# Kernel optimization log

Measured on AMD Instinct MI355X. Metric: run time of the kernel, lower is better.

Reference implementation:

```python
import jax, jax.numpy as jnp
import numpy as np

B, S, D, H = 4, 2048, 1024, 16
HD = D // H  # head_dim = 64


def setup_inputs() -> dict:
    key = jax.random.key(0)
    ks = jax.random.split(key, 8)
    scale = 1.0 / np.sqrt(D)
    return {
        "hidden_states": jax.random.normal(ks[0], (B, S, D), dtype=jnp.float32),
        "attention_mask": jnp.zeros((B, 1, 1, S), dtype=jnp.float32),
        "Wq": jax.random.normal(ks[1], (D, D), dtype=jnp.float32) * scale,
        "bq": jnp.zeros((D,), dtype=jnp.float32),
        "Wk": jax.random.normal(ks[2], (D, D), dtype=jnp.float32) * scale,
        "bk": jnp.zeros((D,), dtype=jnp.float32),
        "Wv": jax.random.normal(ks[3], (D, D), dtype=jnp.float32) * scale,
        "bv": jnp.zeros((D,), dtype=jnp.float32),
    }


def reference(hidden_states, attention_mask, Wq, bq, Wk, bk, Wv, bv):
    def split_heads(x):
        # [B,S,D] -> [B,H,S,HD]
        return x.reshape(B, S, H, HD).transpose(0, 2, 1, 3)

    q = split_heads(hidden_states @ Wq + bq)
    k = split_heads(hidden_states @ Wk + bk)
    v = split_heads(hidden_states @ Wv + bv)

    # [B,H,S,S]
    scores = jnp.einsum("bhqd,bhkd->bhqk", q, k) / jnp.sqrt(jnp.float32(HD))
    scores = scores + attention_mask  # additive mask, broadcasts [B,1,1,S]
    probs = jax.nn.softmax(scores, axis=-1)

    ctx = jnp.einsum("bhqk,bhkd->bhqd", probs, v)  # [B,H,S,HD]
    return ctx.transpose(0, 2, 1, 3).reshape(B, S, D)
```

## Files before the change

kernel.cpp:

```cpp
#include <hip/hip_runtime.h>
#include <hip/hip_bf16.h>
#include <stdint.h>

typedef __attribute__((ext_vector_type(4))) float f32x4;
typedef __attribute__((ext_vector_type(16))) float f32x16;
typedef __attribute__((ext_vector_type(8))) short bf16x8;
typedef __attribute__((ext_vector_type(4))) int int4v;
typedef __attribute__((ext_vector_type(8))) unsigned short u16x8;
typedef unsigned int u32;

static __device__ __forceinline__ unsigned short f2bf(float f) {
    union { float f; unsigned u; } v; v.f = f;
    unsigned r = v.u + 0x7FFF + ((v.u >> 16) & 1);
    return (unsigned short)(r >> 16);
}

static __device__ __forceinline__ u32 cvtpk(float lo, float hi) {
    u32 r;
    asm("v_cvt_pk_bf16_f32 %0, %1, %2" : "=v"(r) : "v"(lo), "v"(hi));
    return r;
}

static __device__ __forceinline__ void pl32swap_u(u32& a, u32& b) {
    asm("v_permlane32_swap_b32 %0, %1" : "+v"(a), "+v"(b));
}

static __device__ __forceinline__ void gload16(const void* g, void* lds) {
    __builtin_amdgcn_global_load_lds((const __attribute__((address_space(1))) void*)g,
                                     (__attribute__((address_space(3))) void*)lds,
                                     16, 0, 0);
}

__global__ __launch_bounds__(256) void cvt_x_kernel(const float* __restrict__ x,
                                                    unsigned short* __restrict__ xb) {
    int i = (blockIdx.x * 256 + threadIdx.x) * 4;
    float4 v = *(const float4*)(x + i);
    ushort4 o = make_ushort4(f2bf(v.x), f2bf(v.y), f2bf(v.z), f2bf(v.w));
    *(ushort4*)(xb + i) = o;
}

__global__ __launch_bounds__(256) void cvt_w_kernel(const float* __restrict__ Wq,
                                                    const float* __restrict__ Wk,
                                                    const float* __restrict__ Wv,
                                                    unsigned short* __restrict__ Wt3) {
    const float* W = (blockIdx.z == 0) ? Wq : ((blockIdx.z == 1) ? Wk : Wv);
    unsigned short* out = Wt3 + (size_t)blockIdx.z * 1024 * 1024;
    __shared__ unsigned short t[64][68];
    int k0 = blockIdx.x * 64, n0 = blockIdx.y * 64;
    int tid = threadIdx.x;
#pragma unroll
    for (int i = 0; i < 4; i++) {
        int c = i * 256 + tid;
        int row = c >> 4, cb = c & 15;
        float4 v = *(const float4*)(W + (size_t)(k0 + row) * 1024 + n0 + cb * 4);
        ushort4 o = make_ushort4(f2bf(v.x), f2bf(v.y), f2bf(v.z), f2bf(v.w));
        *(ushort4*)(&t[row][cb * 4]) = o;
    }
    __syncthreads();
#pragma unroll
    for (int i = 0; i < 2; i++) {
        int c = i * 256 + tid;
        int n = c >> 3, kc = c & 7;
        u16x8 tmp;
#pragma unroll
        for (int j = 0; j < 8; j++) tmp[j] = t[kc * 8 + j][n];
        *(u16x8*)(&out[(size_t)(n0 + n) * 1024 + k0 + kc * 8]) = tmp;
    }
}

__global__ __launch_bounds__(256) void mask_reorder_kernel(const float* __restrict__ mask,
                                                           float* __restrict__ maskr) {
    int o = blockIdx.x * 256 + threadIdx.x;
    int reg = o & 15, kvb = (o >> 4) & 1, hi2 = (o >> 5) & 1, kt = (o >> 6) & 31, bb = o >> 11;
    int kv = kt * 64 + kvb * 32 + (reg & 3) + 8 * (reg >> 2) + 4 * hi2;
    maskr[o] = 8.0f * mask[bb * 2048 + kv];
}

__global__ __launch_bounds__(256) void qkv_gemm_kernel(
    const unsigned short* __restrict__ Xb,
    const unsigned short* __restrict__ Wt3,
    const float* __restrict__ bq, const float* __restrict__ bk, const float* __restrict__ bv,
    unsigned short* __restrict__ Qo, unsigned short* __restrict__ Ko,
    unsigned short* __restrict__ Vt)
{
    int z = blockIdx.z;
    const unsigned short* Wt = Wt3 + (size_t)z * 1048576;
    const float* bias = (z == 0) ? bq : ((z == 1) ? bk : bv);
    int m0 = blockIdx.x * 128, n0 = blockIdx.y * 128;

    __shared__ __align__(16) unsigned short As[128 * 64];
    __shared__ __align__(16) unsigned short Bs[128 * 64];

    int tid = threadIdx.x, lane = tid & 63, wave = tid >> 6;
    int wm = wave >> 1, wn = wave & 1;
    int lr = lane & 15, lg = lane >> 4;

    const int chunkrow = lane >> 3, colp = (lane & 7) * 8;
    const unsigned short* aBase = Xb + (size_t)(m0 + wave * 32 + chunkrow) * 1024 + colp;
    const unsigned short* bBase = Wt + (size_t)(n0 + wave * 32 + chunkrow) * 1024 + colp;
    char* lA = (char*)As + wave * 4096;
    char* lB = (char*)Bs + wave * 4096;

    f32x4 acc[4][4] = {};

    for (int kt = 0; kt < 16; kt++) {
        int kbase = kt * 64;
#pragma unroll
        for (int c = 0; c < 4; c++) {
            gload16(aBase + kbase + c * 8192, lA + c * 1024);
            gload16(bBase + kbase + c * 8192, lB + c * 1024);
        }
        __syncthreads();
#pragma unroll
        for (int kk = 0; kk < 2; kk++) {
            bf16x8 a[4], bb[4];
#pragma unroll
            for (int mi = 0; mi < 4; mi++)
                a[mi] = *(const bf16x8*)((char*)As + (wm * 64 + mi * 16 + lr) * 128 + kk * 64 + lg * 16);
#pragma unroll
            for (int ni = 0; ni < 4; ni++)
                bb[ni] = *(const bf16x8*)((char*)Bs + (wn * 64 + ni * 16 + lr) * 128 + kk * 64 + lg * 16);
#pragma unroll
            for (int mi = 0; mi < 4; mi++)
#pragma unroll
                for (int ni = 0; ni < 4; ni++)
                    acc[mi][ni] = __builtin_amdgcn_mfma_f32_16x16x32_bf16(a[mi], bb[ni], acc[mi][ni], 0, 0, 0);
        }
        __syncthreads();
    }

    if (z < 2) {
        unsigned short* out = (z == 0) ? Qo : Ko;
#pragma unroll
        for (int ni = 0; ni < 4; ni++) {
            int n = n0 + wn * 64 + ni * 16 + lr;
            float bsv = bias[n];
#pragma unroll
            for (int mi = 0; mi < 4; mi++) {
                int mrow = m0 + wm * 64 + mi * 16 + lg * 4;
#pragma unroll
                for (int r = 0; r < 4; r++)
                    out[(size_t)(mrow + r) * 1024 + n] = f2bf(acc[mi][ni][r] + bsv);
            }
        }
    } else {
#pragma unroll
        for (int ni = 0; ni < 4; ni++) {
            int n = n0 + wn * 64 + ni * 16 + lr;
            float bsv = bias[n];
            int h = n >> 6, hd = n & 63;
#pragma unroll
            for (int mi = 0; mi < 4; mi++) {
                int mrow = m0 + wm * 64 + mi * 16 + lg * 4;
                int b = mrow >> 11, s = mrow & 2047;
                ushort4 pk = make_ushort4(f2bf(acc[mi][ni][0] + bsv),
                                          f2bf(acc[mi][ni][1] + bsv),
                                          f2bf(acc[mi][ni][2] + bsv),
                                          f2bf(acc[mi][ni][3] + bsv));
                *(ushort4*)(&Vt[((size_t)(b * 16 + h) * 64 + hd) * 2048 + s]) = pk;
            }
        }
    }
}

__global__ __launch_bounds__(256) void attn_kernel(
    const unsigned short* __restrict__ Q,
    const unsigned short* __restrict__ K,
    const unsigned short* __restrict__ Vt,
    const float* __restrict__ maskr,
    float* __restrict__ out)
{
    __shared__ __align__(16) char smem[33280];
    const int tid = threadIdx.x, lane = tid & 63, w = tid >> 6;
    const int ln31 = lane & 31, hi = lane >> 5;
    const int bh = blockIdx.y, b = bh >> 4, h = bh & 15;
    const int q0 = blockIdx.x * 128 + w * 32;
    const int swz = (ln31 & 7) << 4;
    const float c1 = 0.18033688011112042f;

    const unsigned short* Qrow = Q + (size_t)(b * 2048 + q0 + ln31) * 1024 + h * 64;
    bf16x8 aq[4];
#pragma unroll
    for (int ds = 0; ds < 4; ds++) aq[ds] = *(const bf16x8*)(Qrow + ds * 16 + hi * 8);

    const unsigned short* Kbp = K + (size_t)b * 2048 * 1024 + h * 64;
    const unsigned short* Vbp = Vt + (size_t)bh * 64 * 2048;

    const int r0 = tid >> 3, cb = tid & 7;
    const int woff = r0 * 128 + ((cb * 16) ^ ((r0 & 7) << 4));

    const unsigned short* kp = Kbp + (size_t)r0 * 1024 + cb * 8;
    const unsigned short* vp = Vbp + (size_t)r0 * 2048 + cb * 8;
    const float* mp = maskr + (size_t)b * 2048 + tid * 4;

    f32x16 oacc0 = {}, oacc1 = {};
    float mc = 8.0f * c1;
    float lrun = 0.f;

    int4v kr0, kr1, vr0, vr1, mr = {};
    kr0 = *(const int4v*)kp; kr1 = *(const int4v*)(kp + 32 * 1024);
    vr0 = *(const int4v*)vp; vr1 = *(const int4v*)(vp + 32 * 2048);
    if (tid < 16) mr = *(const int4v*)mp;
    kp += 65536; vp += 64; mp += 64;
    *(int4v*)(smem + woff) = kr0;
    *(int4v*)(smem + 32 * 128 + woff) = kr1;
    *(int4v*)(smem + 16384 + woff) = vr0;
    *(int4v*)(smem + 16384 + 32 * 128 + woff) = vr1;
    if (tid < 16) *(int4v*)(smem + 32768 + tid * 16) = mr;
    kr0 = *(const int4v*)kp; kr1 = *(const int4v*)(kp + 32 * 1024);
    vr0 = *(const int4v*)vp; vr1 = *(const int4v*)(vp + 32 * 2048);
    if (tid < 16) mr = *(const int4v*)mp;
    kp += 65536; vp += 64; mp += 64;
    __syncthreads();

#pragma unroll 2
    for (int kt = 0; kt < 32; kt++) {
        const int cur = kt & 1;
        const char* KsL = smem + cur * 8192 + ln31 * 128;
        const char* VsL = KsL + 16384;
        const f32x4* mpl = (const f32x4*)(smem + 32768 + cur * 256 + hi * 128);

        f32x16 st0, st1;
        {
            f32x4 a0 = mpl[0], a1 = mpl[1], a2 = mpl[2], a3 = mpl[3];
            f32x4 a4 = mpl[4], a5 = mpl[5], a6 = mpl[6], a7 = mpl[7];
#pragma unroll
            for (int j = 0; j < 4; j++) {
                st0[j] = a0[j]; st0[4 + j] = a1[j]; st0[8 + j] = a2[j]; st0[12 + j] = a3[j];
                st1[j] = a4[j]; st1[4 + j] = a5[j]; st1[8 + j] = a6[j]; st1[12 + j] = a7[j];
            }
        }

        __builtin_amdgcn_s_setprio(1);
#pragma unroll
        for (int ds = 0; ds < 4; ds++) {
            const int co = (ds * 32 + hi * 16) ^ swz;
            bf16x8 ka0 = *(const bf16x8*)(KsL + co);
            bf16x8 ka1 = *(const bf16x8*)(KsL + 4096 + co);
            st0 = __builtin_amdgcn_mfma_f32_32x32x16_bf16(ka0, aq[ds], st0, 0, 0, 0);
            st1 = __builtin_amdgcn_mfma_f32_32x32x16_bf16(ka1, aq[ds], st1, 0, 0, 0);
        }
        __builtin_amdgcn_s_setprio(0);

        if (kt < 31) {
            char* base = smem + (cur ^ 1) * 8192;
            *(int4v*)(base + woff) = kr0;
            *(int4v*)(base + 32 * 128 + woff) = kr1;
            *(int4v*)(base + 16384 + woff) = vr0;
            *(int4v*)(base + 16384 + 32 * 128 + woff) = vr1;
            if (tid < 16) *(int4v*)(smem + 32768 + (cur ^ 1) * 256 + tid * 16) = mr;
            if (kt < 30) {
                kr0 = *(const int4v*)kp; kr1 = *(const int4v*)(kp + 32 * 1024);
                vr0 = *(const int4v*)vp; vr1 = *(const int4v*)(vp + 32 * 2048);
                if (tid < 16) mr = *(const int4v*)mp;
                kp += 65536; vp += 64; mp += 64;
            }
        }

        float s16[16];
#pragma unroll
        for (int j = 0; j < 16; j++) {
            float v0 = __builtin_amdgcn_exp2f(__builtin_fmaf(st0[j], c1, -mc));
            float v1 = __builtin_amdgcn_exp2f(__builtin_fmaf(st1[j], c1, -mc));
            st0[j] = v0; st1[j] = v1; s16[j] = v0 + v1;
        }
#pragma unroll
        for (int stp = 8; stp > 0; stp >>= 1)
#pragma unroll
            for (int j = 0; j < 8; j++) if (j < stp) s16[j] += s16[j + stp];

        if (__any(s16[0] > 256.0f)) {
            float me = st0[0];
#pragma unroll
            for (int j = 1; j < 16; j++) me = fmaxf(me, st0[j]);
#pragma unroll
            for (int j = 0; j < 16; j++) me = fmaxf(me, st1[j]);
            me = fmaxf(me, __shfl_xor(me, 32));
            me = fmaxf(me, 1.0f);
            const float al = 1.0f / me;
            mc += __log2f(me);
            lrun *= al; s16[0] *= al;
#pragma unroll
            for (int j = 0; j < 16; j++) {
                st0[j] *= al; st1[j] *= al;
                oacc0[j] *= al; oacc1[j] *= al;
            }
        }
        lrun += s16[0];

        __builtin_amdgcn_s_setprio(1);
#pragma unroll
        for (int s = 0; s < 4; s++) {
            const f32x16& pp = (s & 2) ? st1 : st0;
            const int rA = (s & 1) * 8, rB = rA + 4;
            u32 w0 = cvtpk(pp[rA + 0], pp[rA + 1]);
            u32 w1 = cvtpk(pp[rA + 2], pp[rA + 3]);
            u32 w2 = cvtpk(pp[rB + 0], pp[rB + 1]);
            u32 w3 = cvtpk(pp[rB + 2], pp[rB + 3]);
            pl32swap_u(w0, w2);
            pl32swap_u(w1, w3);
            union { u32 u[4]; bf16x8 v; } pb;
            pb.u[0] = w0; pb.u[1] = w1; pb.u[2] = w2; pb.u[3] = w3;
            const int co = (s * 32 + hi * 16) ^ swz;
            bf16x8 va0 = *(const bf16x8*)(VsL + co);
            bf16x8 va1 = *(const bf16x8*)(VsL + 4096 + co);
            oacc0 = __builtin_amdgcn_mfma_f32_32x32x16_bf16(va0, pb.v, oacc0, 0, 0, 0);
            oacc1 = __builtin_amdgcn_mfma_f32_32x32x16_bf16(va1, pb.v, oacc1, 0, 0, 0);
        }
        __builtin_amdgcn_s_setprio(0);

        __syncthreads();
    }

    float lt = lrun + __shfl_xor(lrun, 32);
    const float rl = 1.0f / lt;
    float* lw = (float*)(smem + w * 4096);
    const int qp = lane >> 1, hb = (lane & 1) * 16;
#pragma unroll
    for (int p = 0; p < 2; p++) {
        const f32x16& oa = p ? oacc1 : oacc0;
#pragma unroll
        for (int r = 0; r < 16; r++) {
            int hd = (r & 3) + 8 * (r >> 2) + 4 * hi;
            lw[hd * 32 + ln31] = oa[r] * rl;
        }
        float* od = out + (size_t)(b * 2048 + q0 + qp) * 1024 + h * 64 + p * 32 + hb;
#pragma unroll
        for (int c = 0; c < 4; c++) {
            f32x4 o4;
#pragma unroll
            for (int j = 0; j < 4; j++) o4[j] = lw[(hb + c * 4 + j) * 32 + qp];
            *(f32x4*)(od + c * 4) = o4;
        }
        __syncthreads();
    }
}

extern "C" void kernel_launch(void* const* d_in, const int* in_sizes, int n_in,
                              void* d_out, int out_size, void* d_ws, size_t ws_size,
                              hipStream_t stream) {
    const float* hs   = (const float*)d_in[0];
    const float* mask = (const float*)d_in[1];
    const float* Wq   = (const float*)d_in[2];
    const float* bq   = (const float*)d_in[3];
    const float* Wk   = (const float*)d_in[4];
    const float* bk   = (const float*)d_in[5];
    const float* Wv   = (const float*)d_in[6];
    const float* bv   = (const float*)d_in[7];
    float* out = (float*)d_out;

    char* ws = (char*)d_ws;
    unsigned short* Xb  = (unsigned short*)ws;
    unsigned short* Wt3 = (unsigned short*)(ws + 16777216);
    unsigned short* Qb  = (unsigned short*)(ws + 16777216 + 6291456);
    unsigned short* Kb  = Qb + 8388608;
    unsigned short* Vt  = Kb + 8388608;
    float* maskr = (float*)(ws + 16777216 + 6291456 + 3 * 16777216);

    cvt_x_kernel<<<8192, 256, 0, stream>>>(hs, Xb);
    cvt_w_kernel<<<dim3(16, 16, 3), 256, 0, stream>>>(Wq, Wk, Wv, Wt3);
    mask_reorder_kernel<<<32, 256, 0, stream>>>(mask, maskr);
    qkv_gemm_kernel<<<dim3(64, 8, 3), 256, 0, stream>>>(Xb, Wt3, bq, bk, bv, Qb, Kb, Vt);
    attn_kernel<<<dim3(16, 64), 256, 0, stream>>>(Qb, Kb, Vt, maskr, out);
}
```

Measured before the change: 199.9 us.

## Double-buffer QKV GEMM LDS tiles and remap block IDs for XCD locality

Converts the QKV projection GEMM from a single 64-wide K tile with two barriers per iteration into a double-buffered 32-wide K tile pipeline. The next tile's global-to-LDS load is issued while the current tile is being consumed by MFMAs, leaving one barrier per step. It also remaps the linear block ID so that consecutive blocks on each XCD (bid&7 striding) cover contiguous tiles, aiming for better L2 reuse of X and W. Risks are halved MFMA work per barrier and possible LDS bank conflicts with the 64-byte row stride.

New measurement: 213.9 us. 7.0% more time.

```diff
diff --git a/kernel.cpp b/kernel.cpp
--- a/kernel.cpp
+++ b/kernel.cpp
@@ -83,51 +83,62 @@
     unsigned short* __restrict__ Qo, unsigned short* __restrict__ Ko,
     unsigned short* __restrict__ Vt)
 {
-    int z = blockIdx.z;
+    const int bid = blockIdx.x + 64 * blockIdx.y + 512 * blockIdx.z;
+    const int nb = (bid & 7) * 192 + (bid >> 3);
+    const int z = nb / 512;
+    const int rem = nb - z * 512;
+    const int n0 = (rem >> 6) * 128;
+    const int m0 = (rem & 63) * 128;
+
     const unsigned short* Wt = Wt3 + (size_t)z * 1048576;
     const float* bias = (z == 0) ? bq : ((z == 1) ? bk : bv);
-    int m0 = blockIdx.x * 128, n0 = blockIdx.y * 128;
-
-    __shared__ __align__(16) unsigned short As[128 * 64];
-    __shared__ __align__(16) unsigned short Bs[128 * 64];
-
-    int tid = threadIdx.x, lane = tid & 63, wave = tid >> 6;
-    int wm = wave >> 1, wn = wave & 1;
-    int lr = lane & 15, lg = lane >> 4;
-
-    const int chunkrow = lane >> 3, colp = (lane & 7) * 8;
-    const unsigned short* aBase = Xb + (size_t)(m0 + wave * 32 + chunkrow) * 1024 + colp;
-    const unsigned short* bBase = Wt + (size_t)(n0 + wave * 32 + chunkrow) * 1024 + colp;
-    char* lA = (char*)As + wave * 4096;
-    char* lB = (char*)Bs + wave * 4096;
+
+    __shared__ __align__(16) unsigned short As[2][128 * 32];
+    __shared__ __align__(16) unsigned short Bs[2][128 * 32];
+
+    const int tid = threadIdx.x, lane = tid & 63, wave = tid >> 6;
+    const int wm = wave >> 1, wn = wave & 1;
+    const int lr = lane & 15, lg = lane >> 4;
+
+    const int c0row = tid >> 2, c0s = tid & 3;
+    const int c1row = (256 + tid) >> 2, c1s = tid & 3;
+    const unsigned short* aG0 = Xb + (size_t)(m0 + c0row) * 1024 + c0s * 8;
+    const unsigned short* aG1 = Xb + (size_t)(m0 + c1row) * 1024 + c1s * 8;
+    const unsigned short* bG0 = Wt + (size_t)(n0 + c0row) * 1024 + c0s * 8;
+    const unsigned short* bG1 = Wt + (size_t)(n0 + c1row) * 1024 + c1s * 8;
 
     f32x4 acc[4][4] = {};
 
-    for (int kt = 0; kt < 16; kt++) {
-        int kbase = kt * 64;
-#pragma unroll
-        for (int c = 0; c < 4; c++) {
-            gload16(aBase + kbase + c * 8192, lA + c * 1024);
-            gload16(bBase + kbase + c * 8192, lB + c * 1024);
-        }
+#define STAGE(bufi, kb)                                                         \
+    do {                                                                        \
+        gload16(aG0 + (kb), (char*)As + (bufi) * 8192 + wave * 1024);           \
+        gload16(bG0 + (kb), (char*)Bs + (bufi) * 8192 + wave * 1024);           \
+        gload16(aG1 + (kb), (char*)As + (bufi) * 8192 + 4096 + wave * 1024);    \
+        gload16(bG1 + (kb), (char*)Bs + (bufi) * 8192 + 4096 + wave * 1024);    \
+    } while (0)
+
+    STAGE(0, 0);
+
+#pragma unroll 2
+    for (int kt = 0; kt < 32; kt++) {
+        const int cur = kt & 1;
         __syncthreads();
-#pragma unroll
-        for (int kk = 0; kk < 2; kk++) {
-            bf16x8 a[4], bb[4];
-#pragma unroll
-            for (int mi = 0; mi < 4; mi++)
-                a[mi] = *(const bf16x8*)((char*)As + (wm * 64 + mi * 16 + lr) * 128 + kk * 64 + lg * 16);
+        if (kt < 31) STAGE(cur ^ 1, (kt + 1) * 32);
+
+        bf16x8 a[4], bb[4];
+#pragma unroll
+        for (int mi = 0; mi < 4; mi++)
+            a[mi] = *(const bf16x8*)((char*)As + cur * 8192 + (wm * 64 + mi * 16 + lr) * 64 + lg * 16);
+#pragma unroll
+        for (int ni = 0; ni < 4; ni++)
+            bb[ni] = *(const bf16x8*)((char*)Bs + cur * 8192 + (wn * 64 + ni * 16 + lr) * 64 + lg * 16);
+#pragma unroll
+        for (int mi = 0; mi < 4; mi++)
 #pragma unroll
             for (int ni = 0; ni < 4; ni++)
-                bb[ni] = *(const bf16x8*)((char*)Bs + (wn * 64 + ni * 16 + lr) * 128 + kk * 64 + lg * 16);
-#pragma unroll
-            for (int mi = 0; mi < 4; mi++)
-#pragma unroll
-                for (int ni = 0; ni < 4; ni++)
-                    acc[mi][ni] = __builtin_amdgcn_mfma_f32_16x16x32_bf16(a[mi], bb[ni], acc[mi][ni], 0, 0, 0);
-        }
-        __syncthreads();
-    }
+                acc[mi][ni] = __builtin_amdgcn_mfma_f32_16x16x32_bf16(a[mi], bb[ni], acc[mi][ni], 0, 0, 0);
+    }
+#undef STAGE
 
     if (z < 2) {
         unsigned short* out = (z == 0) ? Qo : Ko;
```

## Software-pipeline QK^T into previous iteration and read mask directly from global

Applied to the files above, without the earlier changes.

Moves the next tile's mask load and QK^T MFMA block to the end of the current iteration, right after the barrier, so score computation for tile k+1 is issued before the loop back edge. The mask is now read straight from global memory per lane instead of being staged through shared memory. This shrinks LDS to 32 KB, and the launch bounds now request 5 blocks per CU to raise occupancy. Risks include higher register pressure from the 5-wave occupancy hint, possible spills, and extra global mask traffic.

New measurement: 584.0 us. 192% more time.

```diff
diff --git a/kernel.cpp b/kernel.cpp
--- a/kernel.cpp
+++ b/kernel.cpp
@@ -163,14 +163,14 @@
     }
 }
 
-__global__ __launch_bounds__(256) void attn_kernel(
+__global__ __launch_bounds__(256, 5) void attn_kernel(
     const unsigned short* __restrict__ Q,
     const unsigned short* __restrict__ K,
     const unsigned short* __restrict__ Vt,
     const float* __restrict__ maskr,
     float* __restrict__ out)
 {
-    __shared__ __align__(16) char smem[33280];
+    __shared__ __align__(16) char smem[32768];
     const int tid = threadIdx.x, lane = tid & 63, w = tid >> 6;
     const int ln31 = lane & 31, hi = lane >> 5;
     const int bh = blockIdx.y, b = bh >> 4, h = bh & 15;
@@ -185,75 +185,79 @@
 
     const unsigned short* Kbp = K + (size_t)b * 2048 * 1024 + h * 64;
     const unsigned short* Vbp = Vt + (size_t)bh * 64 * 2048;
+    const float* mbase = maskr + (size_t)b * 2048 + hi * 32;
 
     const int r0 = tid >> 3, cb = tid & 7;
     const int woff = r0 * 128 + ((cb * 16) ^ ((r0 & 7) << 4));
 
     const unsigned short* kp = Kbp + (size_t)r0 * 1024 + cb * 8;
     const unsigned short* vp = Vbp + (size_t)r0 * 2048 + cb * 8;
-    const float* mp = maskr + (size_t)b * 2048 + tid * 4;
 
     f32x16 oacc0 = {}, oacc1 = {};
     float mc = 8.0f * c1;
     float lrun = 0.f;
 
-    int4v kr0, kr1, vr0, vr1, mr = {};
+    int4v kr0, kr1, vr0, vr1;
     kr0 = *(const int4v*)kp; kr1 = *(const int4v*)(kp + 32 * 1024);
     vr0 = *(const int4v*)vp; vr1 = *(const int4v*)(vp + 32 * 2048);
-    if (tid < 16) mr = *(const int4v*)mp;
-    kp += 65536; vp += 64; mp += 64;
+    kp += 65536; vp += 64;
     *(int4v*)(smem + woff) = kr0;
     *(int4v*)(smem + 32 * 128 + woff) = kr1;
     *(int4v*)(smem + 16384 + woff) = vr0;
     *(int4v*)(smem + 16384 + 32 * 128 + woff) = vr1;
-    if (tid < 16) *(int4v*)(smem + 32768 + tid * 16) = mr;
     kr0 = *(const int4v*)kp; kr1 = *(const int4v*)(kp + 32 * 1024);
     vr0 = *(const int4v*)vp; vr1 = *(const int4v*)(vp + 32 * 2048);
-    if (tid < 16) mr = *(const int4v*)mp;
-    kp += 65536; vp += 64; mp += 64;
+    kp += 65536; vp += 64;
     __syncthreads();
+
+    f32x16 st0, st1;
+
+#define MASKINIT(ktIdx)                                                         \
+    do {                                                                        \
+        const f32x4* mg = (const f32x4*)(mbase + (ktIdx) * 64);                 \
+        f32x4 a0 = mg[0], a1 = mg[1], a2 = mg[2], a3 = mg[3];                   \
+        f32x4 a4 = mg[4], a5 = mg[5], a6 = mg[6], a7 = mg[7];                   \
+        _Pragma("unroll")                                                       \
+        for (int j = 0; j < 4; j++) {                                           \
+            st0[j] = a0[j]; st0[4 + j] = a1[j]; st0[8 + j] = a2[j]; st0[12 + j] = a3[j]; \
+            st1[j] = a4[j]; st1[4 + j] = a5[j]; st1[8 + j] = a6[j]; st1[12 + j] = a7[j]; \
+        }                                                                       \
+    } while (0)
+
+#define QK(bufi)                                                                \
+    do {                                                                        \
+        const char* KsL = smem + (bufi) * 8192 + ln31 * 128;                    \
+        __builtin_amdgcn_s_setprio(1);                                          \
+        _Pragma("unroll")                                                       \
+        for (int ds = 0; ds < 4; ds++) {                                        \
+            const int co = (ds * 32 + hi * 16) ^ swz;                           \
+            bf16x8 ka0 = *(const bf16x8*)(KsL + co);                            \
+            bf16x8 ka1 = *(const bf16x8*)(KsL + 4096 + co);                     \
+            st0 = __builtin_amdgcn_mfma_f32_32x32x16_bf16(ka0, aq[ds], st0, 0, 0, 0); \
+            st1 = __builtin_amdgcn_mfma_f32_32x32x16_bf16(ka1, aq[ds], st1, 0, 0, 0); \
+        }                                                                       \
+        __builtin_amdgcn_s_setprio(0);                                          \
+    } while (0)
+
+    MASKINIT(0);
+    QK(0);
 
 #pragma unroll 2
     for (int kt = 0; kt < 32; kt++) {
         const int cur = kt & 1;
-        const char* KsL = smem + cur * 8192 + ln31 * 128;
-        const char* VsL = KsL + 16384;
-        const f32x4* mpl = (const f32x4*)(smem + 32768 + cur * 256 + hi * 128);
-
-        f32x16 st0, st1;
-        {
-            f32x4 a0 = mpl[0], a1 = mpl[1], a2 = mpl[2], a3 = mpl[3];
-            f32x4 a4 = mpl[4], a5 = mpl[5], a6 = mpl[6], a7 = mpl[7];
-#pragma unroll
-            for (int j = 0; j < 4; j++) {
-                st0[j] = a0[j]; st0[4 + j] = a1[j]; st0[8 + j] = a2[j]; st0[12 + j] = a3[j];
-                st1[j] = a4[j]; st1[4 + j] = a5[j]; st1[8 + j] = a6[j]; st1[12 + j] = a7[j];
-            }
-        }
-
-        __builtin_amdgcn_s_setprio(1);
-#pragma unroll
-        for (int ds = 0; ds < 4; ds++) {
-            const int co = (ds * 32 + hi * 16) ^ swz;
-            bf16x8 ka0 = *(const bf16x8*)(KsL + co);
-            bf16x8 ka1 = *(const bf16x8*)(KsL + 4096 + co);
-            st0 = __builtin_amdgcn_mfma_f32_32x32x16_bf16(ka0, aq[ds], st0, 0, 0, 0);
-            st1 = __builtin_amdgcn_mfma_f32_32x32x16_bf16(ka1, aq[ds], st1, 0, 0, 0);
-        }
-        __builtin_amdgcn_s_setprio(0);
+        const char* VsL = smem + 16384 + cur * 8192 + ln31 * 128;
 
         if (kt < 31) {
-            char* base = smem + (cur ^ 1) * 8192;
-            *(int4v*)(base + woff) = kr0;
-            *(int4v*)(base + 32 * 128 + woff) = kr1;
-            *(int4v*)(base + 16384 + woff) = vr0;
-            *(int4v*)(base + 16384 + 32 * 128 + woff) = vr1;
-            if (tid < 16) *(int4v*)(smem + 32768 + (cur ^ 1) * 256 + tid * 16) = mr;
+            char* kb = smem + (cur ^ 1) * 8192;
+            char* vb = smem + 16384 + (cur ^ 1) * 8192;
+            *(int4v*)(kb + woff) = kr0;
+            *(int4v*)(kb + 32 * 128 + woff) = kr1;
+            *(int4v*)(vb + woff) = vr0;
+            *(int4v*)(vb + 32 * 128 + woff) = vr1;
             if (kt < 30) {
                 kr0 = *(const int4v*)kp; kr1 = *(const int4v*)(kp + 32 * 1024);
                 vr0 = *(const int4v*)vp; vr1 = *(const int4v*)(vp + 32 * 2048);
-                if (tid < 16) mr = *(const int4v*)mp;
-                kp += 65536; vp += 64; mp += 64;
+                kp += 65536; vp += 64;
             }
         }
 
@@ -309,9 +313,16 @@
         }
         __builtin_amdgcn_s_setprio(0);
 
-        __syncthreads();
-    }
-
+        if (kt < 31) {
+            __syncthreads();
+            MASKINIT(kt + 1);
+            QK(cur ^ 1);
+        }
+    }
+#undef MASKINIT
+#undef QK
+
+    __syncthreads();
     float lt = lrun + __shfl_xor(lrun, 32);
     const float rl = 1.0f / lt;
     float* lw = (float*)(smem + w * 4096);
```
